# Kernel optimization log

Measured on AMD Instinct MI355X. Metric: run time of the kernel, lower is better.

The kernel has to match this reference:

```python
import jax, jax.numpy as jnp
import numpy as np

BN_EPS = 1e-5


def setup_inputs() -> dict:
    key = jax.random.key(0)
    ks = jax.random.split(key, 6)
    N, E, D = 100000, 1600000, 128
    feat = jax.random.normal(ks[0], (N, D), dtype=jnp.float32)
    src = jax.random.randint(ks[1], (E,), 0, N, dtype=jnp.int32)
    dst = jax.random.randint(ks[2], (E,), 0, N, dtype=jnp.int32)
    edge_weight = jax.random.uniform(ks[3], (E,), dtype=jnp.float32)
    # GraphConv linear weight/bias (glorot-ish init)
    W = jax.random.normal(ks[4], (D, D), dtype=jnp.float32) * (1.0 / np.sqrt(D))
    b = jnp.zeros((D,), dtype=jnp.float32)
    # PReLU slopes (nn.PReLU() default single param = 0.25)
    a1 = jnp.full((1,), 0.25, dtype=jnp.float32)
    a2 = jnp.full((1,), 0.25, dtype=jnp.float32)
    # BatchNorm affine params
    gamma = jnp.ones((D,), dtype=jnp.float32)
    beta = jnp.zeros((D,), dtype=jnp.float32)
    return {"feat": feat, "src": src, "dst": dst, "edge_weight": edge_weight,
            "W": W, "b": b, "a1": a1, "gamma": gamma, "beta": beta, "a2": a2}


def _prelu(x, a):
    return jnp.where(x >= 0, x, a * x)


def reference(feat, src, dst, edge_weight, W, b, a1, gamma, beta, a2):
    N = feat.shape[0]
    # Dropout is identity at inference.
    # GraphConv norm='none': edge-weighted neighbor sum (gather-scale-scatter)
    msg = feat[src] * edge_weight[:, None]              # [E, D]
    agg = jax.ops.segment_sum(msg, dst, num_segments=N)  # [N, D]
    h = agg @ W + b                                      # [N, D]
    h = _prelu(h, a1)                                    # conv activation
    # BatchNorm over nodes (training-mode batch stats, biased var)
    mean = h.mean(axis=0)
    var = h.var(axis=0)
    h = (h - mean) / jnp.sqrt(var + BN_EPS) * gamma + beta
    h = _prelu(h, a2)                                    # outer PReLU
    return h
```

## Files before the change

### kernel.cpp

```cpp
#include <hip/hip_runtime.h>

#define D 128
#define BN_EPS 1e-5f
#define CHUNKA 8192
#define NBCAP 512
#define MAXSEGH 3072

typedef __attribute__((ext_vector_type(8))) short bf16x8;
typedef __attribute__((ext_vector_type(8))) unsigned short u16x8;
typedef __attribute__((ext_vector_type(4))) float f32x4;

__device__ __forceinline__ unsigned short f2bf(float f) {
    unsigned int u = __float_as_uint(f);
    u += 0x7FFFu + ((u >> 16) & 1u);
    return (unsigned short)(u >> 16);
}
__device__ __forceinline__ float bf2f(unsigned short u) {
    return __uint_as_float(((unsigned int)u) << 16);
}

__global__ __launch_bounds__(256) void prep_w_kernel(
    const float* __restrict__ W, unsigned short* __restrict__ wswz)
{
    int i = blockIdx.x * 256 + threadIdx.x;
    int j  = i & 7;
    int l  = (i >> 3) & 63;
    int c  = (i >> 9) & 7;
    int ks = i >> 12;
    int k   = ks * 32 + ((l >> 4) * 8) + j;
    int col = c * 16 + (l & 15);
    wswz[i] = f2bf(W[k * D + col]);
}

__global__ __launch_bounds__(512) void init_bcur_kernel(
    int* __restrict__ bcur, int NB, int CAP)
{
    int t = threadIdx.x;
    if (t < NB) bcur[t] = t * CAP;
}

__global__ __launch_bounds__(1024) void partition_feat_kernel(
    const int* __restrict__ src, const int* __restrict__ dst,
    const float* __restrict__ ew, int* __restrict__ bcur,
    int2* __restrict__ csr,
    const float* __restrict__ feat, unsigned short* __restrict__ featb,
    long n8, int E, int NB, int CAP)
{
    __shared__ int2 sedge[CHUNKA];
    __shared__ unsigned short sbkt[CHUNKA];
    __shared__ int lcnt[NBCAP];
    __shared__ int lstart[NBCAP];
    __shared__ int lcur[NBCAP];
    __shared__ int gbase[NBCAP];
    int t = threadIdx.x;
    int bid = blockIdx.x;
    int nchunks = gridDim.x / 3;
    int rem = bid % 3;
    if (rem != 0) {
        long fb = (long)(bid / 3) * 2 + (rem - 1);
        long i = fb * 1024 + t;
        long stride = (long)(2 * nchunks) * 1024;
        for (; i < n8; i += stride) {
            float4 a = *reinterpret_cast<const float4*>(feat + i * 8);
            float4 b = *reinterpret_cast<const float4*>(feat + i * 8 + 4);
            u16x8 o;
            o[0] = f2bf(a.x); o[1] = f2bf(a.y); o[2] = f2bf(a.z); o[3] = f2bf(a.w);
            o[4] = f2bf(b.x); o[5] = f2bf(b.y); o[6] = f2bf(b.z); o[7] = f2bf(b.w);
            reinterpret_cast<u16x8*>(featb)[i] = o;
        }
        return;
    }
    int base = (bid / 3) * CHUNKA;
    int lim = min(CHUNKA, E - base);
    for (int k = t; k < NB; k += 1024) lcnt[k] = 0;
    __syncthreads();
    int dv[8]; int sv[8]; float wv[8];
    #pragma unroll
    for (int j = 0; j < 8; ++j) {
        int idx = base + j * 1024 + t;
        bool ok = (j * 1024 + t) < lim;
        dv[j] = ok ? dst[idx] : -1;
        sv[j] = ok ? src[idx] : 0;
        wv[j] = ok ? ew[idx] : 0.f;
        if (ok) atomicAdd(&lcnt[dv[j] >> 8], 1);
    }
    __syncthreads();
    {
        int v = (t < NB) ? lcnt[t] : 0;
        if (t < 512) lstart[t] = (t < NB) ? v : 0;
        __syncthreads();
        for (int d = 1; d < 512; d <<= 1) {
            int val = (t < 512 && t >= d) ? lstart[t - d] : 0;
            __syncthreads();
            if (t < 512) lstart[t] += val;
            __syncthreads();
        }
        if (t < NB) {
            int excl = lstart[t] - v;
            lcur[t] = excl;
            gbase[t] = (v > 0) ? atomicAdd(&bcur[t], v) : 0;
        }
        __syncthreads();
        if (t < NB) lstart[t] = lcur[t];
        __syncthreads();
    }
    #pragma unroll
    for (int j = 0; j < 8; ++j) {
        if (dv[j] >= 0) {
            int b = dv[j] >> 8;
            int p = atomicAdd(&lcur[b], 1);
            sedge[p] = make_int2((sv[j] & 0xFFFFF) | ((dv[j] & 255) << 20),
                                 __float_as_int(wv[j]));
            sbkt[p] = (unsigned short)b;
        }
    }
    __syncthreads();
    for (int p = t; p < lim; p += 1024) {
        int b = sbkt[p];
        int dest = gbase[b] + (p - lstart[b]);
        if (dest < (b + 1) * CAP)
            csr[dest] = sedge[p];
    }
}

__global__ __launch_bounds__(512) void bucket_sort_agg_kernel(
    const unsigned short* __restrict__ featb, const int2* __restrict__ csr,
    const int* __restrict__ bcur, unsigned short* __restrict__ aggb,
    int N, int CAP)
{
    __shared__ int   lsrc[MAXSEGH];
    __shared__ float lwf[MAXSEGH];
    __shared__ int cnt[128];
    __shared__ int nstart[128];
    __shared__ int ncur[128];
    int t = threadIdx.x;
    int k = blockIdx.x >> 1;
    int h = blockIdx.x & 1;
    int segbeg = k * CAP;
    int len = bcur[k] - segbeg;
    if (len > CAP) len = CAP;
    int segend = segbeg + len;
    long nlo = ((long)k << 8) + (h << 7);
    if (t < 128) cnt[t] = 0;
    __syncthreads();
    for (int j = segbeg + t; j < segend; j += 512) {
        int s = (csr[j].x >> 20) & 255;
        if ((s >> 7) == h) atomicAdd(&cnt[s & 127], 1);
    }
    __syncthreads();
    int v = (t < 128) ? cnt[t] : 0;
    if (t < 128) nstart[t] = v;
    __syncthreads();
    for (int d = 1; d < 128; d <<= 1) {
        int val = (t >= d && t < 128) ? nstart[t - d] : 0;
        __syncthreads();
        if (t < 128) nstart[t] += val;
        __syncthreads();
    }
    int total = nstart[127];
    __syncthreads();
    if (t < 128) { int e = nstart[t] - v; nstart[t] = e; ncur[t] = e; }
    __syncthreads();

    int g = t >> 4;
    int q = (t & 15) << 3;

    if (total <= MAXSEGH) {
        for (int j = segbeg + t; j < segend; j += 512) {
            int2 e = csr[j];
            int s = (e.x >> 20) & 255;
            if ((s >> 7) == h) {
                int p = atomicAdd(&ncur[s & 127], 1);
                lsrc[p] = e.x & 0xFFFFF;
                lwf[p]  = __int_as_float(e.y);
            }
        }
        __syncthreads();
        #pragma unroll
        for (int r = 0; r < 4; ++r) {
            int n = r * 32 + g;
            int beg = nstart[n];
            int end = ncur[n];
            float acc0[8] = {0.f,0.f,0.f,0.f,0.f,0.f,0.f,0.f};
            float acc1[8] = {0.f,0.f,0.f,0.f,0.f,0.f,0.f,0.f};
            int i = beg;
            for (; i + 2 <= end; i += 2) {
                int s0 = lsrc[i], s1 = lsrc[i + 1];
                float w0 = lwf[i], w1 = lwf[i + 1];
                u16x8 v0 = *reinterpret_cast<const u16x8*>(featb + (long)s0 * D + q);
                u16x8 v1 = *reinterpret_cast<const u16x8*>(featb + (long)s1 * D + q);
                #pragma unroll
                for (int jj = 0; jj < 8; ++jj) {
                    acc0[jj] += bf2f(v0[jj]) * w0;
                    acc1[jj] += bf2f(v1[jj]) * w1;
                }
            }
            if (i < end) {
                int s0 = lsrc[i];
                float w0 = lwf[i];
                u16x8 v0 = *reinterpret_cast<const u16x8*>(featb + (long)s0 * D + q);
                #pragma unroll
                for (int jj = 0; jj < 8; ++jj) acc0[jj] += bf2f(v0[jj]) * w0;
            }
            long row = nlo + n;
            if (row < N) {
                u16x8 o;
                #pragma unroll
                for (int jj = 0; jj < 8; ++jj) o[jj] = f2bf(acc0[jj] + acc1[jj]);
                *reinterpret_cast<u16x8*>(aggb + row * D + q) = o;
            }
        }
    } else {
        #pragma unroll
        for (int r = 0; r < 4; ++r) {
            int n = r * 32 + g;
            int target = (h << 7) | n;
            float acc[8] = {0.f,0.f,0.f,0.f,0.f,0.f,0.f,0.f};
            for (int j = segbeg; j < segend; ++j) {
                int2 e = csr[j];
                if (((e.x >> 20) & 255) == target) {
                    float w = __int_as_float(e.y);
                    u16x8 vv = *reinterpret_cast<const u16x8*>(
                        featb + (long)(e.x & 0xFFFFF) * D + q);
                    #pragma unroll
                    for (int jj = 0; jj < 8; ++jj) acc[jj] += bf2f(vv[jj]) * w;
                }
            }
            long row = nlo + n;
            if (row < N) {
                u16x8 o;
                #pragma unroll
                for (int jj = 0; jj < 8; ++jj) o[jj] = f2bf(acc[jj]);
                *reinterpret_cast<u16x8*>(aggb + row * D + q) = o;
            }
        }
    }
}

__global__ __launch_bounds__(256) void gemm_stats_mfma_kernel(
    const unsigned short* aggb, const unsigned short* __restrict__ wswz,
    const float* __restrict__ bg, const float* __restrict__ a1p,
    unsigned short* houtb, float* __restrict__ stats, int N)
{
    __shared__ unsigned short Bl[16384];
    __shared__ float sblk[2][D];

    int t = threadIdx.x;
    for (int i = t; i < 2048; i += 256)
        reinterpret_cast<float4*>(Bl)[i] = reinterpret_cast<const float4*>(wswz)[i];
    if (t < D) { sblk[0][t] = 0.f; sblk[1][t] = 0.f; }
    __syncthreads();

    const int lane = t & 63;
    const int wv   = t >> 6;
    const long rbase = (long)blockIdx.x * 128 + wv * 32;
    const int lr = lane & 15;
    const int lk = lane >> 4;

    f32x4 acc[2][8];
    #pragma unroll
    for (int rt = 0; rt < 2; ++rt)
        #pragma unroll
        for (int c = 0; c < 8; ++c)
            acc[rt][c] = (f32x4){0.f, 0.f, 0.f, 0.f};

    long r0 = rbase + lr;
    long r1 = rbase + 16 + lr;
    long r0c = (r0 < N) ? r0 : 0;
    long r1c = (r1 < N) ? r1 : 0;

    #pragma unroll
    for (int ks = 0; ks < 4; ++ks) {
        bf16x8 a0 = *reinterpret_cast<const bf16x8*>(aggb + r0c * D + ks * 32 + lk * 8);
        bf16x8 a1f = *reinterpret_cast<const bf16x8*>(aggb + r1c * D + ks * 32 + lk * 8);
        #pragma unroll
        for (int c = 0; c < 8; ++c) {
            bf16x8 bfr = *reinterpret_cast<const bf16x8*>(&Bl[((ks * 8 + c) * 64 + lane) * 8]);
            acc[0][c] = __builtin_amdgcn_mfma_f32_16x16x32_bf16(a0, bfr, acc[0][c], 0, 0, 0);
            acc[1][c] = __builtin_amdgcn_mfma_f32_16x16x32_bf16(a1f, bfr, acc[1][c], 0, 0, 0);
        }
    }

    const float a1v = a1p[0];
    float bias[8];
    #pragma unroll
    for (int c = 0; c < 8; ++c) bias[c] = bg[c * 16 + lr];

    float csum[8] = {0,0,0,0,0,0,0,0};
    float csq[8]  = {0,0,0,0,0,0,0,0};
    #pragma unroll
    for (int rt = 0; rt < 2; ++rt) {
        #pragma unroll
        for (int reg = 0; reg < 4; ++reg) {
            long row = rbase + rt * 16 + lk * 4 + reg;
            if (row >= N) continue;
            #pragma unroll
            for (int c = 0; c < 8; ++c) {
                float v = acc[rt][c][reg] + bias[c];
                v = v >= 0.f ? v : v * a1v;
                houtb[row * D + c * 16 + lr] = f2bf(v);
                csum[c] += v;
                csq[c]  += v * v;
            }
        }
    }
    #pragma unroll
    for (int c = 0; c < 8; ++c) {
        atomicAdd(&sblk[0][c * 16 + lr], csum[c]);
        atomicAdd(&sblk[1][c * 16 + lr], csq[c]);
    }
    __syncthreads();
    if (t < D) {
        atomicAdd(&stats[t],     sblk[0][t]);
        atomicAdd(&stats[D + t], sblk[1][t]);
    }
}

__global__ void finalize_kernel(const float* __restrict__ stats,
                                const float* __restrict__ gamma,
                                const float* __restrict__ beta,
                                float* __restrict__ ss, int N)
{
    int c = threadIdx.x;
    float invN = 1.0f / (float)N;
    float mean = stats[c] * invN;
    float var  = stats[D + c] * invN - mean * mean;
    float sc = gamma[c] * rsqrtf(var + BN_EPS);
    ss[c]     = sc;
    ss[D + c] = beta[c] - mean * sc;
}

__global__ __launch_bounds__(256) void bn_prelu_bf16_kernel(
    const unsigned short* __restrict__ hb, const float* __restrict__ ss,
    const float* __restrict__ a2, float* __restrict__ out, long n8)
{
    const float a2v = a2[0];
    long i = (long)blockIdx.x * blockDim.x + threadIdx.x;
    long stride = (long)gridDim.x * blockDim.x;
    for (; i < n8; i += stride) {
        u16x8 hv = reinterpret_cast<const u16x8*>(hb)[i];
        int c0 = ((int)i & 15) << 3;
        float4 sc0 = *reinterpret_cast<const float4*>(ss + c0);
        float4 sc1 = *reinterpret_cast<const float4*>(ss + c0 + 4);
        float4 sh0 = *reinterpret_cast<const float4*>(ss + D + c0);
        float4 sh1 = *reinterpret_cast<const float4*>(ss + D + c0 + 4);
        float4 o0, o1;
        float v;
        v = bf2f(hv[0]) * sc0.x + sh0.x; o0.x = v >= 0.f ? v : v * a2v;
        v = bf2f(hv[1]) * sc0.y + sh0.y; o0.y = v >= 0.f ? v : v * a2v;
        v = bf2f(hv[2]) * sc0.z + sh0.z; o0.z = v >= 0.f ? v : v * a2v;
        v = bf2f(hv[3]) * sc0.w + sh0.w; o0.w = v >= 0.f ? v : v * a2v;
        v = bf2f(hv[4]) * sc1.x + sh1.x; o1.x = v >= 0.f ? v : v * a2v;
        v = bf2f(hv[5]) * sc1.y + sh1.y; o1.y = v >= 0.f ? v : v * a2v;
        v = bf2f(hv[6]) * sc1.z + sh1.z; o1.z = v >= 0.f ? v : v * a2v;
        v = bf2f(hv[7]) * sc1.w + sh1.w; o1.w = v >= 0.f ? v : v * a2v;
        *reinterpret_cast<float4*>(out + i * 8)     = o0;
        *reinterpret_cast<float4*>(out + i * 8 + 4) = o1;
    }
}

__global__ __launch_bounds__(256) void scatter_kernel(
    const float* __restrict__ feat, const int* __restrict__ src,
    const int* __restrict__ dst, const float* __restrict__ ew,
    float* __restrict__ agg, int E)
{
    long tid = (long)blockIdx.x * blockDim.x + threadIdx.x;
    int e = (int)(tid >> 5);
    if (e >= E) return;
    int q = ((int)tid & 31) << 2;
    int s = src[e];
    int d = dst[e];
    float w = ew[e];
    float4 v = *reinterpret_cast<const float4*>(feat + (long)s * D + q);
    float* o = agg + (long)d * D + q;
    atomicAdd(o + 0, v.x * w);
    atomicAdd(o + 1, v.y * w);
    atomicAdd(o + 2, v.z * w);
    atomicAdd(o + 3, v.w * w);
}

__global__ __launch_bounds__(256) void gemm_stats_kernel(
    const float* __restrict__ agg, const float* __restrict__ Wg,
    const float* __restrict__ bg, const float* __restrict__ a1,
    float* __restrict__ hout, float* __restrict__ stats, int N)
{
    __shared__ float Wl[D * D];
    __shared__ float sblk[2][D];

    int t = threadIdx.x;
    for (int i = t; i < D * D / 4; i += 256) {
        reinterpret_cast<float4*>(Wl)[i] =
            reinterpret_cast<const float4*>(Wg)[i];
    }
    if (t < D) { sblk[0][t] = 0.f; sblk[1][t] = 0.f; }
    __syncthreads();

    const int c0 = (t & 31) << 2;
    const int rbase = blockIdx.x * 32 + (t >> 5) * 4;
    const float a1v = a1[0];

    bool valid[4];
    #pragma unroll
    for (int i = 0; i < 4; ++i) valid[i] = (rbase + i) < N;

    float acc[4][4];
    float4 bv = *reinterpret_cast<const float4*>(bg + c0);
    #pragma unroll
    for (int i = 0; i < 4; ++i) {
        acc[i][0] = bv.x; acc[i][1] = bv.y; acc[i][2] = bv.z; acc[i][3] = bv.w;
    }

    for (int k0 = 0; k0 < D; k0 += 4) {
        float4 a[4];
        #pragma unroll
        for (int i = 0; i < 4; ++i) {
            a[i] = valid[i]
                ? *reinterpret_cast<const float4*>(agg + (long)(rbase + i) * D + k0)
                : make_float4(0.f, 0.f, 0.f, 0.f);
        }
        #pragma unroll
        for (int kk = 0; kk < 4; ++kk) {
            float4 wv = *reinterpret_cast<const float4*>(&Wl[(k0 + kk) * D + c0]);
            #pragma unroll
            for (int i = 0; i < 4; ++i) {
                float av = kk == 0 ? a[i].x : kk == 1 ? a[i].y : kk == 2 ? a[i].z : a[i].w;
                acc[i][0] += av * wv.x;
                acc[i][1] += av * wv.y;
                acc[i][2] += av * wv.z;
                acc[i][3] += av * wv.w;
            }
        }
    }

    float csum[4] = {0.f, 0.f, 0.f, 0.f};
    float csq[4]  = {0.f, 0.f, 0.f, 0.f};
    #pragma unroll
    for (int i = 0; i < 4; ++i) {
        if (!valid[i]) continue;
        float4 o;
        #pragma unroll
        for (int j = 0; j < 4; ++j) {
            float v = acc[i][j];
            v = v >= 0.f ? v : v * a1v;
            (&o.x)[j] = v;
            csum[j] += v;
            csq[j]  += v * v;
        }
        *reinterpret_cast<float4*>(hout + (long)(rbase + i) * D + c0) = o;
    }
    #pragma unroll
    for (int j = 0; j < 4; ++j) {
        atomicAdd(&sblk[0][c0 + j], csum[j]);
        atomicAdd(&sblk[1][c0 + j], csq[j]);
    }
    __syncthreads();
    if (t < D) {
        atomicAdd(&stats[t],     sblk[0][t]);
        atomicAdd(&stats[D + t], sblk[1][t]);
    }
}

__global__ __launch_bounds__(256) void bn_prelu_kernel(
    float* __restrict__ h, const float* __restrict__ ss,
    const float* __restrict__ a2, long n4)
{
    const float a2v = a2[0];
    long i = (long)blockIdx.x * blockDim.x + threadIdx.x;
    long stride = (long)gridDim.x * blockDim.x;
    for (; i < n4; i += stride) {
        float4 x = reinterpret_cast<float4*>(h)[i];
        int c0 = ((int)(i & 31)) << 2;
        float4 sc = *reinterpret_cast<const float4*>(ss + c0);
        float4 sh = *reinterpret_cast<const float4*>(ss + D + c0);
        float v;
        v = x.x * sc.x + sh.x; x.x = v >= 0.f ? v : v * a2v;
        v = x.y * sc.y + sh.y; x.y = v >= 0.f ? v : v * a2v;
        v = x.z * sc.z + sh.z; x.z = v >= 0.f ? v : v * a2v;
        v = x.w * sc.w + sh.w; x.w = v >= 0.f ? v : v * a2v;
        reinterpret_cast<float4*>(h)[i] = x;
    }
}

extern "C" void kernel_launch(void* const* d_in, const int* in_sizes, int n_in,
                              void* d_out, int out_size, void* d_ws, size_t ws_size,
                              hipStream_t stream)
{
    const float* feat  = (const float*)d_in[0];
    const int*   src   = (const int*)d_in[1];
    const int*   dst   = (const int*)d_in[2];
    const float* ew    = (const float*)d_in[3];
    const float* W     = (const float*)d_in[4];
    const float* b     = (const float*)d_in[5];
    const float* a1    = (const float*)d_in[6];
    const float* gamma = (const float*)d_in[7];
    const float* beta  = (const float*)d_in[8];
    const float* a2    = (const float*)d_in[9];

    const int N = in_sizes[0] / D;
    const int E = in_sizes[1];

    int NB = (N + 255) / 256;
    int mean = (NB > 0) ? (E / NB) : 0;
    int margin = mean / 4; if (margin < 1024) margin = 1024;
    int CAP = ((mean + margin) + 3) & ~3;

    char* p = (char*)d_ws;
    unsigned short* featb = (unsigned short*)p; p += (size_t)N * D * sizeof(unsigned short);
    unsigned short* aggb  = (unsigned short*)p; p += (size_t)N * D * sizeof(unsigned short);
    int2* csr = (int2*)p;                 p += (size_t)NB * CAP * sizeof(int2);
    int*   bcur  = (int*)p;               p += NBCAP * sizeof(int);
    float* stats = (float*)p;             p += 2 * D * sizeof(float);
    unsigned short* wswz = (unsigned short*)p; p += 16384 * sizeof(unsigned short);
    float* ss    = (float*)p;             p += 2 * D * sizeof(float);
    size_t need = (size_t)(p - (char*)d_ws);
    float* out = (float*)d_out;

    if (ws_size >= need && NB <= NBCAP) {
        hipMemsetAsync(stats, 0, 2 * D * sizeof(float), stream);
        prep_w_kernel<<<64, 256, 0, stream>>>(W, wswz);
        init_bcur_kernel<<<1, 512, 0, stream>>>(bcur, NB, CAP);
        long n8 = (long)N * D / 8;
        int nchunks = (E + CHUNKA - 1) / CHUNKA;
        partition_feat_kernel<<<3 * nchunks, 1024, 0, stream>>>(
            src, dst, ew, bcur, csr, feat, featb, n8, E, NB, CAP);
        bucket_sort_agg_kernel<<<2 * NB, 512, 0, stream>>>(featb, csr, bcur, aggb, N, CAP);
        int gblocks = (N + 127) / 128;
        gemm_stats_mfma_kernel<<<gblocks, 256, 0, stream>>>(aggb, wswz, b, a1, aggb, stats, N);
        finalize_kernel<<<1, D, 0, stream>>>(stats, gamma, beta, ss, N);
        bn_prelu_bf16_kernel<<<2048, 256, 0, stream>>>(aggb, ss, a2, out, n8);
    } else {
        float* agg = (float*)d_ws;
        stats = agg + (size_t)N * D;
        ss    = stats + 2 * D;
        hipMemsetAsync(agg, 0, ((size_t)N * D + 2 * D) * sizeof(float), stream);
        long nthreads = (long)E * 32;
        int sblocks = (int)((nthreads + 255) / 256);
        scatter_kernel<<<sblocks, 256, 0, stream>>>(feat, src, dst, ew, agg, E);
        int gblocks = (N + 31) / 32;
        gemm_stats_kernel<<<gblocks, 256, 0, stream>>>(agg, W, b, a1, out, stats, N);
        finalize_kernel<<<1, D, 0, stream>>>(stats, gamma, beta, ss, N);
        long n4 = (long)N * D / 4;
        bn_prelu_kernel<<<2048, 256, 0, stream>>>(out, ss, a2, n4);
    }
}
```

Baseline: 171.0 us.

## Shrink destination buckets from 256 to 64 nodes for partition and aggregation

Changes the destination-node bucketing from 256 to 64 nodes per bucket, which gives about four times as many buckets. Each aggregation block now handles one 64-node bucket with 256 threads, so it no longer splits a bucket in half and scans every edge twice. The partition kernel widens its per-block scan to cover up to 2048 buckets, with each thread handling two buckets. The cost is more global atomics on bucket cursors and more scattered CSR writes during partitioning, in exchange for less redundant edge reading in aggregation.

```diff
diff --git a/kernel.cpp b/kernel.cpp
--- a/kernel.cpp
+++ b/kernel.cpp
@@ -3,8 +3,9 @@
 #define D 128
 #define BN_EPS 1e-5f
 #define CHUNKA 8192
-#define NBCAP 512
-#define MAXSEGH 3072
+#define BKT 64
+#define NBCAP2 2048
+#define MAXSEGB 2048
 
 typedef __attribute__((ext_vector_type(8))) short bf16x8;
 typedef __attribute__((ext_vector_type(8))) unsigned short u16x8;
@@ -32,11 +33,11 @@
     wswz[i] = f2bf(W[k * D + col]);
 }
 
-__global__ __launch_bounds__(512) void init_bcur_kernel(
+__global__ __launch_bounds__(256) void init_bcur_kernel(
     int* __restrict__ bcur, int NB, int CAP)
 {
-    int t = threadIdx.x;
-    if (t < NB) bcur[t] = t * CAP;
+    int k = blockIdx.x * 256 + threadIdx.x;
+    if (k < NB) bcur[k] = k * CAP;
 }
 
 __global__ __launch_bounds__(1024) void partition_feat_kernel(
@@ -48,10 +49,11 @@
 {
     __shared__ int2 sedge[CHUNKA];
     __shared__ unsigned short sbkt[CHUNKA];
-    __shared__ int lcnt[NBCAP];
-    __shared__ int lstart[NBCAP];
-    __shared__ int lcur[NBCAP];
-    __shared__ int gbase[NBCAP];
+    __shared__ int lcnt[NBCAP2];
+    __shared__ int lstart[NBCAP2];
+    __shared__ int lcur[NBCAP2];
+    __shared__ int gbase[NBCAP2];
+    __shared__ int part[1024];
     int t = threadIdx.x;
     int bid = blockIdx.x;
     int nchunks = gridDim.x / 3;
@@ -82,34 +84,39 @@
         dv[j] = ok ? dst[idx] : -1;
         sv[j] = ok ? src[idx] : 0;
         wv[j] = ok ? ew[idx] : 0.f;
-        if (ok) atomicAdd(&lcnt[dv[j] >> 8], 1);
+        if (ok) atomicAdd(&lcnt[dv[j] >> 6], 1);
     }
     __syncthreads();
     {
-        int v = (t < NB) ? lcnt[t] : 0;
-        if (t < 512) lstart[t] = (t < NB) ? v : 0;
+        int b0 = 2 * t, b1 = 2 * t + 1;
+        int v0 = (b0 < NB) ? lcnt[b0] : 0;
+        int v1 = (b1 < NB) ? lcnt[b1] : 0;
+        part[t] = v0 + v1;
         __syncthreads();
-        for (int d = 1; d < 512; d <<= 1) {
-            int val = (t < 512 && t >= d) ? lstart[t - d] : 0;
+        for (int d = 1; d < 1024; d <<= 1) {
+            int val = (t >= d) ? part[t - d] : 0;
             __syncthreads();
-            if (t < 512) lstart[t] += val;
+            part[t] += val;
             __syncthreads();
         }
-        if (t < NB) {
-            int excl = lstart[t] - v;
-            lcur[t] = excl;
-            gbase[t] = (v > 0) ? atomicAdd(&bcur[t], v) : 0;
-        }
-        __syncthreads();
-        if (t < NB) lstart[t] = lcur[t];
+        int run = part[t] - (v0 + v1);
+        if (b0 < NB) {
+            lstart[b0] = run; lcur[b0] = run;
+            gbase[b0] = (v0 > 0) ? atomicAdd(&bcur[b0], v0) : 0;
+        }
+        if (b1 < NB) {
+            int e1 = run + v0;
+            lstart[b1] = e1; lcur[b1] = e1;
+            gbase[b1] = (v1 > 0) ? atomicAdd(&bcur[b1], v1) : 0;
+        }
         __syncthreads();
     }
     #pragma unroll
     for (int j = 0; j < 8; ++j) {
         if (dv[j] >= 0) {
-            int b = dv[j] >> 8;
+            int b = dv[j] >> 6;
             int p = atomicAdd(&lcur[b], 1);
-            sedge[p] = make_int2((sv[j] & 0xFFFFF) | ((dv[j] & 255) << 20),
+            sedge[p] = make_int2((sv[j] & 0xFFFFF) | ((dv[j] & 63) << 20),
                                  __float_as_int(wv[j]));
             sbkt[p] = (unsigned short)b;
         }
@@ -123,62 +130,55 @@
     }
 }
 
-__global__ __launch_bounds__(512) void bucket_sort_agg_kernel(
+__global__ __launch_bounds__(256) void bucket_sort_agg_kernel(
     const unsigned short* __restrict__ featb, const int2* __restrict__ csr,
     const int* __restrict__ bcur, unsigned short* __restrict__ aggb,
     int N, int CAP)
 {
-    __shared__ int   lsrc[MAXSEGH];
-    __shared__ float lwf[MAXSEGH];
-    __shared__ int cnt[128];
-    __shared__ int nstart[128];
-    __shared__ int ncur[128];
+    __shared__ int   lsrc[MAXSEGB];
+    __shared__ float lwf[MAXSEGB];
+    __shared__ int cnt[BKT];
+    __shared__ int nstart[BKT];
+    __shared__ int ncur[BKT];
     int t = threadIdx.x;
-    int k = blockIdx.x >> 1;
-    int h = blockIdx.x & 1;
+    int k = blockIdx.x;
     int segbeg = k * CAP;
     int len = bcur[k] - segbeg;
     if (len > CAP) len = CAP;
     int segend = segbeg + len;
-    long nlo = ((long)k << 8) + (h << 7);
-    if (t < 128) cnt[t] = 0;
-    __syncthreads();
-    for (int j = segbeg + t; j < segend; j += 512) {
-        int s = (csr[j].x >> 20) & 255;
-        if ((s >> 7) == h) atomicAdd(&cnt[s & 127], 1);
-    }
-    __syncthreads();
-    int v = (t < 128) ? cnt[t] : 0;
-    if (t < 128) nstart[t] = v;
-    __syncthreads();
-    for (int d = 1; d < 128; d <<= 1) {
-        int val = (t >= d && t < 128) ? nstart[t - d] : 0;
+    long nlo = (long)k * BKT;
+    if (t < BKT) cnt[t] = 0;
+    __syncthreads();
+    for (int j = segbeg + t; j < segend; j += 256)
+        atomicAdd(&cnt[(csr[j].x >> 20) & 63], 1);
+    __syncthreads();
+    int v = (t < BKT) ? cnt[t] : 0;
+    if (t < BKT) nstart[t] = v;
+    __syncthreads();
+    for (int d = 1; d < BKT; d <<= 1) {
+        int val = (t >= d && t < BKT) ? nstart[t - d] : 0;
         __syncthreads();
-        if (t < 128) nstart[t] += val;
+        if (t < BKT) nstart[t] += val;
         __syncthreads();
     }
-    int total = nstart[127];
-    __syncthreads();
-    if (t < 128) { int e = nstart[t] - v; nstart[t] = e; ncur[t] = e; }
+    __syncthreads();
+    if (t < BKT) { int e = nstart[t] - v; nstart[t] = e; ncur[t] = e; }
     __syncthreads();
 
     int g = t >> 4;
     int q = (t & 15) << 3;
 
-    if (total <= MAXSEGH) {
-        for (int j = segbeg + t; j < segend; j += 512) {
+    if (len <= MAXSEGB) {
+        for (int j = segbeg + t; j < segend; j += 256) {
             int2 e = csr[j];
-            int s = (e.x >> 20) & 255;
-            if ((s >> 7) == h) {
-                int p = atomicAdd(&ncur[s & 127], 1);
-                lsrc[p] = e.x & 0xFFFFF;
-                lwf[p]  = __int_as_float(e.y);
-            }
+            int p = atomicAdd(&ncur[(e.x >> 20) & 63], 1);
+            lsrc[p] = e.x & 0xFFFFF;
+            lwf[p]  = __int_as_float(e.y);
         }
         __syncthreads();
         #pragma unroll
         for (int r = 0; r < 4; ++r) {
-            int n = r * 32 + g;
+            int n = r * 16 + g;
             int beg = nstart[n];
             int end = ncur[n];
             float acc0[8] = {0.f,0.f,0.f,0.f,0.f,0.f,0.f,0.f};
@@ -213,12 +213,11 @@
     } else {
         #pragma unroll
         for (int r = 0; r < 4; ++r) {
-            int n = r * 32 + g;
-            int target = (h << 7) | n;
+            int n = r * 16 + g;
             float acc[8] = {0.f,0.f,0.f,0.f,0.f,0.f,0.f,0.f};
             for (int j = segbeg; j < segend; ++j) {
                 int2 e = csr[j];
-                if (((e.x >> 20) & 255) == target) {
+                if (((e.x >> 20) & 63) == n) {
                     float w = __int_as_float(e.y);
                     u16x8 vv = *reinterpret_cast<const u16x8*>(
                         featb + (long)(e.x & 0xFFFFF) * D + q);
@@ -499,31 +498,31 @@
     const int N = in_sizes[0] / D;
     const int E = in_sizes[1];
 
-    int NB = (N + 255) / 256;
+    int NB = (N + BKT - 1) / BKT;
     int mean = (NB > 0) ? (E / NB) : 0;
-    int margin = mean / 4; if (margin < 1024) margin = 1024;
+    int margin = mean / 4; if (margin < 320) margin = 320;
     int CAP = ((mean + margin) + 3) & ~3;
 
     char* p = (char*)d_ws;
     unsigned short* featb = (unsigned short*)p; p += (size_t)N * D * sizeof(unsigned short);
     unsigned short* aggb  = (unsigned short*)p; p += (size_t)N * D * sizeof(unsigned short);
     int2* csr = (int2*)p;                 p += (size_t)NB * CAP * sizeof(int2);
-    int*   bcur  = (int*)p;               p += NBCAP * sizeof(int);
+    int*   bcur  = (int*)p;               p += NBCAP2 * sizeof(int);
     float* stats = (float*)p;             p += 2 * D * sizeof(float);
     unsigned short* wswz = (unsigned short*)p; p += 16384 * sizeof(unsigned short);
     float* ss    = (float*)p;             p += 2 * D * sizeof(float);
     size_t need = (size_t)(p - (char*)d_ws);
     float* out = (float*)d_out;
 
-    if (ws_size >= need && NB <= NBCAP) {
+    if (ws_size >= need && NB <= NBCAP2) {
         hipMemsetAsync(stats, 0, 2 * D * sizeof(float), stream);
         prep_w_kernel<<<64, 256, 0, stream>>>(W, wswz);
-        init_bcur_kernel<<<1, 512, 0, stream>>>(bcur, NB, CAP);
+        init_bcur_kernel<<<(NB + 255) / 256, 256, 0, stream>>>(bcur, NB, CAP);
         long n8 = (long)N * D / 8;
         int nchunks = (E + CHUNKA - 1) / CHUNKA;
         partition_feat_kernel<<<3 * nchunks, 1024, 0, stream>>>(
             src, dst, ew, bcur, csr, feat, featb, n8, E, NB, CAP);
-        bucket_sort_agg_kernel<<<2 * NB, 512, 0, stream>>>(featb, csr, bcur, aggb, N, CAP);
+        bucket_sort_agg_kernel<<<NB, 256, 0, stream>>>(featb, csr, bcur, aggb, N, CAP);
         int gblocks = (N + 127) / 128;
         gemm_stats_mfma_kernel<<<gblocks, 256, 0, stream>>>(aggb, wswz, b, a1, aggb, stats, N);
         finalize_kernel<<<1, D, 0, stream>>>(stats, gamma, beta, ss, N);
```

Measured after the change: 160.3 us. 6.3% less time.
